# Kernel optimization log

Hardware: AMD Instinct MI355X
Metric: run time of the kernel (lower is better)

The kernel has to match this reference:

```python
import jax, jax.numpy as jnp
import numpy as np

LOG2 = 0.6931471805599453

def ssp(x):
    # shifted softplus, SchNet's standard activation
    return jax.nn.softplus(x) - LOG2

def setup_inputs() -> dict:
    key = jax.random.key(0)
    ks = jax.random.split(key, 8)
    B, A, N, G, F = 8, 1024, 64, 50, 128
    s = lambda fan_in: 1.0 / np.sqrt(fan_in)
    return {
        "x": jax.random.normal(ks[0], (B, A, F), jnp.float32),
        "pairwise_mask": jnp.ones((B, A, N), jnp.float32),
        "neighbors": jax.random.randint(ks[1], (B, A, N), 0, A),
        "f_ij": jax.random.uniform(ks[2], (B, A, N, G), jnp.float32),
        "W_f1": jax.random.normal(ks[3], (G, F), jnp.float32) * s(G),
        "b_f1": jnp.zeros((F,), jnp.float32),
        "W_f2": jax.random.normal(ks[4], (F, F), jnp.float32) * s(F),
        "b_f2": jnp.zeros((F,), jnp.float32),
        "W_in2f": jax.random.normal(ks[5], (F, F), jnp.float32) * s(F),
        "W_f2out": jax.random.normal(ks[6], (F, F), jnp.float32) * s(F),
        "b_f2out": jnp.zeros((F,), jnp.float32),
    }

def reference(x, pairwise_mask, neighbors, f_ij, W_f1, b_f1, W_f2, b_f2,
              W_in2f, W_f2out, b_f2out):
    B, A, N = neighbors.shape
    # filter network: Dense+ssp then Dense (no activation) -> [B,A,N,F]
    W = ssp(jnp.einsum('bang,gf->banf', f_ij, W_f1) + b_f1)
    W = jnp.einsum('banf,fk->bank', W, W_f2) + b_f2
    # neighbor gather: x[b, neighbors[b,a,n], :] -> [B,A,N,C]
    nbh = neighbors.reshape(B, A * N, 1)           # [B, A*N, 1]
    x_nbh = jnp.take_along_axis(x, nbh, axis=1)    # broadcast over C -> [B, A*N, C]
    x_nbh = x_nbh.reshape(B, A, N, -1)
    # in2f dense (no bias), filter multiply, masked sum over neighbor axis
    y = jnp.einsum('banc,cf->banf', x_nbh, W_in2f)
    y = y * W
    y = jnp.sum(y * pairwise_mask[..., None], axis=2)  # [B, A, F]
    # f2out dense with shifted-softplus activation
    y = ssp(jnp.einsum('baf,fo->bao', y, W_f2out) + b_f2out)
    return y
```

## Files before the change

### kernel.cpp

```cpp
#include <hip/hip_runtime.h>

#define B_ 8
#define A_ 1024
#define N_ 64
#define G_ 50
#define F_ 128
#define ATOMS 4

typedef __attribute__((ext_vector_type(8))) short bf16x8;
typedef __attribute__((ext_vector_type(4))) float f32x4;

__device__ __forceinline__ float sspf(float v) {
    return fmaxf(v, 0.f) + __logf(1.f + __expf(-fabsf(v))) - 0.69314718055994530942f;
}
__device__ __forceinline__ unsigned short f2bf(float f) {
    unsigned u = __float_as_uint(f);
    u += 0x7fffu + ((u >> 16) & 1u);
    return (unsigned short)(u >> 16);
}
__device__ __forceinline__ unsigned cvt_pk(float lo, float hi) {
    unsigned r;
    asm("v_cvt_pk_bf16_f32 %0, %1, %2" : "=v"(r) : "v"(lo), "v"(hi));
    return r;
}
__device__ __forceinline__ float red16(float p) {
    p += __int_as_float(__builtin_amdgcn_ds_swizzle(__float_as_int(p), 0x041F));
    p += __int_as_float(__builtin_amdgcn_ds_swizzle(__float_as_int(p), 0x081F));
    p += __int_as_float(__builtin_amdgcn_ds_swizzle(__float_as_int(p), 0x101F));
    p += __int_as_float(__builtin_amdgcn_ds_swizzle(__float_as_int(p), 0x201F));
    return p;
}

__global__ __launch_bounds__(256) void pack_all(
    const float* __restrict__ W1, const float* __restrict__ b1,
    const float* __restrict__ W2, const float* __restrict__ Wi,
    const float* __restrict__ Wo,
    unsigned short* __restrict__ P1, unsigned short* __restrict__ P2,
    unsigned short* __restrict__ Pi, unsigned short* __restrict__ Po)
{
    int blk = blockIdx.x;
    const float* W; const float* bias = nullptr; unsigned short* P; int K, id;
    if (blk < 32)       { W = W1; P = P1; K = 50;  id = blk * 256 + threadIdx.x; bias = b1; }
    else if (blk < 96)  { W = W2; P = P2; K = 128; id = (blk - 32) * 256 + threadIdx.x; }
    else if (blk < 160) { W = Wi; P = Pi; K = 128; id = (blk - 96) * 256 + threadIdx.x; }
    else                { W = Wo; P = Po; K = 128; id = (blk - 160) * 256 + threadIdx.x; }
    int i    = id & 7;
    int lane = (id >> 3) & 63;
    int nt   = (id >> 9) & 7;
    int ks   = id >> 12;
    int k = 32 * ks + 8 * (lane >> 4) + i;
    int f = 16 * nt + (lane & 15);
    float v = (k < K) ? W[k * F_ + f] : ((bias && k == K) ? bias[f] : 0.f);
    P[id] = f2bf(v);
}

template <bool ACT, bool OUT_BF16>
__global__ __launch_bounds__(64) void rowgemm_kernel(
    const float* Afp, const unsigned short* __restrict__ Bp,
    const float* __restrict__ bias, void* outv)
{
    const int l  = threadIdx.x;
    const int r0 = blockIdx.x * 16;
    const bf16x8* Bv = (const bf16x8*)Bp;

    f32x4 acc[8];
    #pragma unroll
    for (int nt = 0; nt < 8; ++nt) acc[nt] = f32x4{0.f, 0.f, 0.f, 0.f};

    const int arow = r0 + (l & 15);
    const int koff = (l >> 4) * 8;
    #pragma unroll
    for (int ks = 0; ks < 4; ++ks) {
        const float* ap = Afp + (size_t)arow * F_ + ks * 32 + koff;
        float4 a0 = *(const float4*)ap;
        float4 a1 = *(const float4*)(ap + 4);
        bf16x8 af;
        af[0] = (short)f2bf(a0.x); af[1] = (short)f2bf(a0.y);
        af[2] = (short)f2bf(a0.z); af[3] = (short)f2bf(a0.w);
        af[4] = (short)f2bf(a1.x); af[5] = (short)f2bf(a1.y);
        af[6] = (short)f2bf(a1.z); af[7] = (short)f2bf(a1.w);
        #pragma unroll
        for (int nt = 0; nt < 8; ++nt) {
            bf16x8 bf = Bv[(ks * 8 + nt) * 64 + l];
            acc[nt] = __builtin_amdgcn_mfma_f32_16x16x32_bf16(af, bf, acc[nt], 0, 0, 0);
        }
    }
    #pragma unroll
    for (int nt = 0; nt < 8; ++nt) {
        int f = nt * 16 + (l & 15);
        float bv = bias ? bias[f] : 0.f;
        #pragma unroll
        for (int r = 0; r < 4; ++r) {
            int orow = r0 + (l >> 4) * 4 + r;
            float v = acc[nt][r] + bv;
            if (ACT) v = sspf(v);
            if (OUT_BF16) ((unsigned short*)outv)[(size_t)orow * F_ + f] = f2bf(v);
            else          ((float*)outv)[(size_t)orow * F_ + f] = v;
        }
    }
}

__global__ __launch_bounds__(256, 3) void cfconv_main(
    const unsigned short* __restrict__ xt,
    const float* __restrict__ mask,
    const int*   __restrict__ nbr,
    const float* __restrict__ fij,
    const unsigned short* __restrict__ W1s,
    const unsigned short* __restrict__ W2s,
    const float* __restrict__ bf2,
    float* __restrict__ Y)
{
    const int ba0 = blockIdx.x * ATOMS;
    const int b   = ba0 >> 10;
    const int t   = threadIdx.x;
    const int w   = t >> 6;
    const int l   = t & 63;
    const int l16 = l & 15;
    const int q   = l >> 4;

    __shared__ unsigned short s_fp[2][4096];
    __shared__ unsigned short s_hp[8192];

    const bf16x8* w1v = (const bf16x8*)W1s;
    const bf16x8* w2v = (const bf16x8*)W2s;
    bf16x8 W1r[2][2], W2r[4][2];
    #pragma unroll
    for (int ks = 0; ks < 2; ++ks) {
        W1r[ks][0] = w1v[(ks * 8 + 2 * w + 0) * 64 + l];
        W1r[ks][1] = w1v[(ks * 8 + 2 * w + 1) * 64 + l];
    }
    #pragma unroll
    for (int ks = 0; ks < 4; ++ks) {
        W2r[ks][0] = w2v[(ks * 8 + 2 * w + 0) * 64 + l];
        W2r[ks][1] = w2v[(ks * 8 + 2 * w + 1) * 64 + l];
    }
    float4 b2r[2];
    b2r[0] = *(const float4*)(bf2 + 16 * (2 * w + 0) + 4 * q);
    b2r[1] = *(const float4*)(bf2 + 16 * (2 * w + 1) + 4 * q);

    int nbv[4]; float mkv[4];
    #pragma unroll
    for (int nt = 0; nt < 4; ++nt) {
        nbv[nt] = nbr[(size_t)ba0 * N_ + 16 * nt + l16];
        mkv[nt] = mask[(size_t)ba0 * N_ + 16 * nt + l16];
    }
    float2 fa[4], fb[4];
    {
        const float* frow = fij + (size_t)ba0 * (N_ * G_) + (16 * w + l16) * G_;
        #pragma unroll
        for (int j = 0; j < 4; ++j) fa[j] = *(const float2*)(frow + 8 * q + 2 * j);
        if (q < 2) {
            #pragma unroll
            for (int j = 0; j < 4; ++j) fb[j] = *(const float2*)(frow + 32 + 8 * q + 2 * j);
        } else if (q == 2) {
            fb[0] = *(const float2*)(frow + 48);
            fb[1] = float2{1.f, 0.f};
            fb[2] = float2{0.f, 0.f}; fb[3] = float2{0.f, 0.f};
        } else {
            #pragma unroll
            for (int j = 0; j < 4; ++j) fb[j] = float2{0.f, 0.f};
        }
    }
    uint2 xg[2][4];
    #pragma unroll
    for (int f2 = 0; f2 < 2; ++f2) {
        const int f0 = 16 * (2 * w + f2) + 4 * q;
        #pragma unroll
        for (int nt = 0; nt < 4; ++nt)
            xg[f2][nt] = *(const uint2*)(xt + ((size_t)(b << 10) + nbv[nt]) * F_ + f0);
    }
    {
        uint4 pk0, pk1;
        pk0.x = cvt_pk(fa[0].x, fa[0].y); pk0.y = cvt_pk(fa[1].x, fa[1].y);
        pk0.z = cvt_pk(fa[2].x, fa[2].y); pk0.w = cvt_pk(fa[3].x, fa[3].y);
        pk1.x = cvt_pk(fb[0].x, fb[0].y); pk1.y = cvt_pk(fb[1].x, fb[1].y);
        pk1.z = cvt_pk(fb[2].x, fb[2].y); pk1.w = cvt_pk(fb[3].x, fb[3].y);
        *(uint4*)(&s_fp[0][((w * 2 + 0) * 64 + l) * 8]) = pk0;
        *(uint4*)(&s_fp[0][((w * 2 + 1) * 64 + l) * 8]) = pk1;
    }
    __syncthreads();

    int nbv2[4]; float mkv2[4];

    #pragma unroll
    for (int i = 0; i < ATOMS; ++i) {
        const int ba = ba0 + i;
        const unsigned short* fp_cur = s_fp[i & 1];
        unsigned short* fp_nxt = s_fp[(i + 1) & 1];

        const bf16x8* fv = (const bf16x8*)fp_cur;
        f32x4 acc1[2][4];
        #pragma unroll
        for (int c = 0; c < 2; ++c)
            #pragma unroll
            for (int nt = 0; nt < 4; ++nt) acc1[c][nt] = f32x4{0.f, 0.f, 0.f, 0.f};
        #pragma unroll
        for (int ks = 0; ks < 2; ++ks) {
            bf16x8 bb[4];
            #pragma unroll
            for (int nt = 0; nt < 4; ++nt) bb[nt] = fv[(nt * 2 + ks) * 64 + l];
            #pragma unroll
            for (int nt = 0; nt < 4; ++nt) {
                acc1[0][nt] = __builtin_amdgcn_mfma_f32_16x16x32_bf16(W1r[ks][0], bb[nt], acc1[0][nt], 0, 0, 0);
                acc1[1][nt] = __builtin_amdgcn_mfma_f32_16x16x32_bf16(W1r[ks][1], bb[nt], acc1[1][nt], 0, 0, 0);
            }
        }

        if (i < ATOMS - 1) {
            const float* frow = fij + (size_t)(ba + 1) * (N_ * G_) + (16 * w + l16) * G_;
            #pragma unroll
            for (int j = 0; j < 4; ++j) fa[j] = *(const float2*)(frow + 8 * q + 2 * j);
            if (q < 2) {
                #pragma unroll
                for (int j = 0; j < 4; ++j) fb[j] = *(const float2*)(frow + 32 + 8 * q + 2 * j);
            } else if (q == 2) {
                fb[0] = *(const float2*)(frow + 48);
                fb[1] = float2{1.f, 0.f};
                fb[2] = float2{0.f, 0.f}; fb[3] = float2{0.f, 0.f};
            } else {
                #pragma unroll
                for (int j = 0; j < 4; ++j) fb[j] = float2{0.f, 0.f};
            }
            #pragma unroll
            for (int nt = 0; nt < 4; ++nt) {
                nbv2[nt] = nbr[(size_t)(ba + 1) * N_ + 16 * nt + l16];
                mkv2[nt] = mask[(size_t)(ba + 1) * N_ + 16 * nt + l16];
            }
        }

        #pragma unroll
        for (int ct2 = 0; ct2 < 2; ++ct2) {
            const int addr = ((w * 64 + 16 * (2 * ct2 + (q >> 1)) + l16) * 8 + 4 * (q & 1));
            #pragma unroll
            for (int nt = 0; nt < 4; ++nt) {
                float h0 = sspf(acc1[ct2][nt][0]);
                float h1 = sspf(acc1[ct2][nt][1]);
                float h2 = sspf(acc1[ct2][nt][2]);
                float h3 = sspf(acc1[ct2][nt][3]);
                uint2 pk;
                pk.x = cvt_pk(h0, h1);
                pk.y = cvt_pk(h2, h3);
                *(uint2*)(&s_hp[nt * 2048 + addr]) = pk;
            }
        }

        if (i < ATOMS - 1) {
            uint4 pk0, pk1;
            pk0.x = cvt_pk(fa[0].x, fa[0].y); pk0.y = cvt_pk(fa[1].x, fa[1].y);
            pk0.z = cvt_pk(fa[2].x, fa[2].y); pk0.w = cvt_pk(fa[3].x, fa[3].y);
            pk1.x = cvt_pk(fb[0].x, fb[0].y); pk1.y = cvt_pk(fb[1].x, fb[1].y);
            pk1.z = cvt_pk(fb[2].x, fb[2].y); pk1.w = cvt_pk(fb[3].x, fb[3].y);
            *(uint4*)(&fp_nxt[((w * 2 + 0) * 64 + l) * 8]) = pk0;
            *(uint4*)(&fp_nxt[((w * 2 + 1) * 64 + l) * 8]) = pk1;
        }
        __syncthreads();

        const bf16x8* hv = (const bf16x8*)s_hp;
        f32x4 acc2[2][4];
        #pragma unroll
        for (int c = 0; c < 2; ++c)
            #pragma unroll
            for (int nt = 0; nt < 4; ++nt) acc2[c][nt] = f32x4{0.f, 0.f, 0.f, 0.f};
        #pragma unroll
        for (int ks = 0; ks < 4; ++ks) {
            bf16x8 bb[4];
            #pragma unroll
            for (int nt = 0; nt < 4; ++nt) bb[nt] = hv[(nt * 4 + ks) * 64 + l];
            #pragma unroll
            for (int nt = 0; nt < 4; ++nt) {
                acc2[0][nt] = __builtin_amdgcn_mfma_f32_16x16x32_bf16(W2r[ks][0], bb[nt], acc2[0][nt], 0, 0, 0);
                acc2[1][nt] = __builtin_amdgcn_mfma_f32_16x16x32_bf16(W2r[ks][1], bb[nt], acc2[1][nt], 0, 0, 0);
            }
        }

        #pragma unroll
        for (int f2 = 0; f2 < 2; ++f2) {
            const float4 b2v = b2r[f2];
            float p0 = 0.f, p1 = 0.f, p2 = 0.f, p3 = 0.f;
            #pragma unroll
            for (int nt = 0; nt < 4; ++nt) {
                const float msk = mkv[nt];
                const uint2 xv = xg[f2][nt];
                const float x0 = __uint_as_float(xv.x << 16);
                const float x1 = __uint_as_float(xv.x & 0xffff0000u);
                const float x2 = __uint_as_float(xv.y << 16);
                const float x3 = __uint_as_float(xv.y & 0xffff0000u);
                p0 = fmaf(msk * (acc2[f2][nt][0] + b2v.x), x0, p0);
                p1 = fmaf(msk * (acc2[f2][nt][1] + b2v.y), x1, p1);
                p2 = fmaf(msk * (acc2[f2][nt][2] + b2v.z), x2, p2);
                p3 = fmaf(msk * (acc2[f2][nt][3] + b2v.w), x3, p3);
            }
            p0 = red16(p0); p1 = red16(p1); p2 = red16(p2); p3 = red16(p3);
            if (l16 == 0)
                *(float4*)(Y + (size_t)ba * F_ + 16 * (2 * w + f2) + 4 * q) = float4{p0, p1, p2, p3};
        }

        if (i < ATOMS - 1) {
            #pragma unroll
            for (int nt = 0; nt < 4; ++nt) { nbv[nt] = nbv2[nt]; mkv[nt] = mkv2[nt]; }
            #pragma unroll
            for (int f2 = 0; f2 < 2; ++f2) {
                const int f0 = 16 * (2 * w + f2) + 4 * q;
                #pragma unroll
                for (int nt = 0; nt < 4; ++nt)
                    xg[f2][nt] = *(const uint2*)(xt + ((size_t)(b << 10) + nbv[nt]) * F_ + f0);
            }
        }
        __syncthreads();
    }
}

extern "C" void kernel_launch(void* const* d_in, const int* in_sizes, int n_in,
                              void* d_out, int out_size, void* d_ws, size_t ws_size,
                              hipStream_t stream) {
    const float* x     = (const float*)d_in[0];
    const float* mask  = (const float*)d_in[1];
    const int*   nbr   = (const int*)d_in[2];
    const float* fij   = (const float*)d_in[3];
    const float* Wf1   = (const float*)d_in[4];
    const float* bf1   = (const float*)d_in[5];
    const float* Wf2   = (const float*)d_in[6];
    const float* bf2   = (const float*)d_in[7];
    const float* Win2f = (const float*)d_in[8];
    const float* Wout  = (const float*)d_in[9];
    const float* bout  = (const float*)d_in[10];
    float* out = (float*)d_out;

    char* ws = (char*)d_ws;
    unsigned short* W1p   = (unsigned short*)(ws);
    unsigned short* W2p   = (unsigned short*)(ws + 16384);
    unsigned short* Winp  = (unsigned short*)(ws + 49152);
    unsigned short* Woutp = (unsigned short*)(ws + 81920);
    unsigned short* xt    = (unsigned short*)(ws + 114688);

    pack_all<<<224, 256, 0, stream>>>(Wf1, bf1, Wf2, Win2f, Wout, W1p, W2p, Winp, Woutp);

    rowgemm_kernel<false, true><<<B_ * A_ / 16, 64, 0, stream>>>(x, Winp, nullptr, xt);

    cfconv_main<<<B_ * A_ / ATOMS, 256, 0, stream>>>(xt, mask, nbr, fij, W1p, W2p, bf2, out);

    rowgemm_kernel<true, false><<<B_ * A_ / 16, 64, 0, stream>>>(out, Woutp, bout, out);
}
```

Measured before the change: 91.83 us.

## Raise occupancy, single-buffer filter LDS, swizzle blocks, fold bias into MFMA, add setprio

Raises the launch-bounds occupancy hint from 3 to 5 waves and halves the f_ij LDS staging by using a single buffer, which needs an extra barrier between the layer-1 MFMAs and the overwrite. Blocks are remapped with an XCD-style swizzle (bid&7) so that neighboring atoms go to the same die, aiming at better L2 locality for the gathered x rows. The bias b_f2 now initialises the second GEMM's MFMA accumulator instead of being added in the epilogue, and the first k-step seeds with zero so no accumulators need clearing. s_setprio wraps the MFMA sections, and address math is simplified. The tighter register budget may cause spills.

```diff
diff --git a/kernel.cpp b/kernel.cpp
--- a/kernel.cpp
+++ b/kernel.cpp
@@ -100,7 +100,7 @@
     }
 }
 
-__global__ __launch_bounds__(256, 3) void cfconv_main(
+__global__ __launch_bounds__(256, 5) void cfconv_main(
     const unsigned short* __restrict__ xt,
     const float* __restrict__ mask,
     const int*   __restrict__ nbr,
@@ -110,16 +110,20 @@
     const float* __restrict__ bf2,
     float* __restrict__ Y)
 {
-    const int ba0 = blockIdx.x * ATOMS;
-    const int b   = ba0 >> 10;
+    const int bid = blockIdx.x;
+    const int swz = (bid & 7) * (2048 / 8) + (bid >> 3);
+    const int ba0 = swz * ATOMS;
     const int t   = threadIdx.x;
     const int w   = t >> 6;
     const int l   = t & 63;
     const int l16 = l & 15;
     const int q   = l >> 4;
 
-    __shared__ unsigned short s_fp[2][4096];
+    __shared__ unsigned short s_fp[4096];
     __shared__ unsigned short s_hp[8192];
+
+    const unsigned short* xt_b = xt + ((size_t)(ba0 >> 10) << 10) * F_;
+    const int xoff = 32 * w + 4 * q;
 
     const bf16x8* w1v = (const bf16x8*)W1s;
     const bf16x8* w2v = (const bf16x8*)W2s;
@@ -134,15 +138,23 @@
         W2r[ks][0] = w2v[(ks * 8 + 2 * w + 0) * 64 + l];
         W2r[ks][1] = w2v[(ks * 8 + 2 * w + 1) * 64 + l];
     }
-    float4 b2r[2];
-    b2r[0] = *(const float4*)(bf2 + 16 * (2 * w + 0) + 4 * q);
-    b2r[1] = *(const float4*)(bf2 + 16 * (2 * w + 1) + 4 * q);
+    f32x4 b2acc[2];
+    {
+        float4 t0 = *(const float4*)(bf2 + 16 * (2 * w + 0) + 4 * q);
+        float4 t1 = *(const float4*)(bf2 + 16 * (2 * w + 1) + 4 * q);
+        b2acc[0] = f32x4{t0.x, t0.y, t0.z, t0.w};
+        b2acc[1] = f32x4{t1.x, t1.y, t1.z, t1.w};
+    }
 
     int nbv[4]; float mkv[4];
-    #pragma unroll
-    for (int nt = 0; nt < 4; ++nt) {
-        nbv[nt] = nbr[(size_t)ba0 * N_ + 16 * nt + l16];
-        mkv[nt] = mask[(size_t)ba0 * N_ + 16 * nt + l16];
+    {
+        const int*   nb0 = nbr  + (size_t)ba0 * N_;
+        const float* mk0 = mask + (size_t)ba0 * N_;
+        #pragma unroll
+        for (int nt = 0; nt < 4; ++nt) {
+            nbv[nt] = nb0[16 * nt + l16];
+            mkv[nt] = mk0[16 * nt + l16];
+        }
     }
     float2 fa[4], fb[4];
     {
@@ -163,20 +175,18 @@
     }
     uint2 xg[2][4];
     #pragma unroll
-    for (int f2 = 0; f2 < 2; ++f2) {
-        const int f0 = 16 * (2 * w + f2) + 4 * q;
+    for (int f2 = 0; f2 < 2; ++f2)
         #pragma unroll
         for (int nt = 0; nt < 4; ++nt)
-            xg[f2][nt] = *(const uint2*)(xt + ((size_t)(b << 10) + nbv[nt]) * F_ + f0);
-    }
+            xg[f2][nt] = *(const uint2*)(xt_b + nbv[nt] * F_ + xoff + 16 * f2);
     {
         uint4 pk0, pk1;
         pk0.x = cvt_pk(fa[0].x, fa[0].y); pk0.y = cvt_pk(fa[1].x, fa[1].y);
         pk0.z = cvt_pk(fa[2].x, fa[2].y); pk0.w = cvt_pk(fa[3].x, fa[3].y);
         pk1.x = cvt_pk(fb[0].x, fb[0].y); pk1.y = cvt_pk(fb[1].x, fb[1].y);
         pk1.z = cvt_pk(fb[2].x, fb[2].y); pk1.w = cvt_pk(fb[3].x, fb[3].y);
-        *(uint4*)(&s_fp[0][((w * 2 + 0) * 64 + l) * 8]) = pk0;
-        *(uint4*)(&s_fp[0][((w * 2 + 1) * 64 + l) * 8]) = pk1;
+        *(uint4*)(&s_fp[((w * 2 + 0) * 64 + l) * 8]) = pk0;
+        *(uint4*)(&s_fp[((w * 2 + 1) * 64 + l) * 8]) = pk1;
     }
     __syncthreads();
 
@@ -185,26 +195,28 @@
     #pragma unroll
     for (int i = 0; i < ATOMS; ++i) {
         const int ba = ba0 + i;
-        const unsigned short* fp_cur = s_fp[i & 1];
-        unsigned short* fp_nxt = s_fp[(i + 1) & 1];
-
-        const bf16x8* fv = (const bf16x8*)fp_cur;
+
+        const bf16x8* fv = (const bf16x8*)s_fp;
         f32x4 acc1[2][4];
-        #pragma unroll
-        for (int c = 0; c < 2; ++c)
-            #pragma unroll
-            for (int nt = 0; nt < 4; ++nt) acc1[c][nt] = f32x4{0.f, 0.f, 0.f, 0.f};
-        #pragma unroll
-        for (int ks = 0; ks < 2; ++ks) {
+        __builtin_amdgcn_s_setprio(1);
+        {
             bf16x8 bb[4];
             #pragma unroll
-            for (int nt = 0; nt < 4; ++nt) bb[nt] = fv[(nt * 2 + ks) * 64 + l];
-            #pragma unroll
-            for (int nt = 0; nt < 4; ++nt) {
-                acc1[0][nt] = __builtin_amdgcn_mfma_f32_16x16x32_bf16(W1r[ks][0], bb[nt], acc1[0][nt], 0, 0, 0);
-                acc1[1][nt] = __builtin_amdgcn_mfma_f32_16x16x32_bf16(W1r[ks][1], bb[nt], acc1[1][nt], 0, 0, 0);
-            }
-        }
+            for (int nt = 0; nt < 4; ++nt) bb[nt] = fv[(nt * 2 + 0) * 64 + l];
+            #pragma unroll
+            for (int nt = 0; nt < 4; ++nt) {
+                acc1[0][nt] = __builtin_amdgcn_mfma_f32_16x16x32_bf16(W1r[0][0], bb[nt], f32x4{0.f,0.f,0.f,0.f}, 0, 0, 0);
+                acc1[1][nt] = __builtin_amdgcn_mfma_f32_16x16x32_bf16(W1r[0][1], bb[nt], f32x4{0.f,0.f,0.f,0.f}, 0, 0, 0);
+            }
+            #pragma unroll
+            for (int nt = 0; nt < 4; ++nt) bb[nt] = fv[(nt * 2 + 1) * 64 + l];
+            #pragma unroll
+            for (int nt = 0; nt < 4; ++nt) {
+                acc1[0][nt] = __builtin_amdgcn_mfma_f32_16x16x32_bf16(W1r[1][0], bb[nt], acc1[0][nt], 0, 0, 0);
+                acc1[1][nt] = __builtin_amdgcn_mfma_f32_16x16x32_bf16(W1r[1][1], bb[nt], acc1[1][nt], 0, 0, 0);
+            }
+        }
+        __builtin_amdgcn_s_setprio(0);
 
         if (i < ATOMS - 1) {
             const float* frow = fij + (size_t)(ba + 1) * (N_ * G_) + (16 * w + l16) * G_;
@@ -221,10 +233,12 @@
                 #pragma unroll
                 for (int j = 0; j < 4; ++j) fb[j] = float2{0.f, 0.f};
             }
-            #pragma unroll
-            for (int nt = 0; nt < 4; ++nt) {
-                nbv2[nt] = nbr[(size_t)(ba + 1) * N_ + 16 * nt + l16];
-                mkv2[nt] = mask[(size_t)(ba + 1) * N_ + 16 * nt + l16];
+            const int*   nb1 = nbr  + (size_t)(ba + 1) * N_;
+            const float* mk1 = mask + (size_t)(ba + 1) * N_;
+            #pragma unroll
+            for (int nt = 0; nt < 4; ++nt) {
+                nbv2[nt] = nb1[16 * nt + l16];
+                mkv2[nt] = mk1[16 * nt + l16];
             }
         }
 
@@ -243,6 +257,7 @@
                 *(uint2*)(&s_hp[nt * 2048 + addr]) = pk;
             }
         }
+        __syncthreads();
 
         if (i < ATOMS - 1) {
             uint4 pk0, pk1;
@@ -250,32 +265,37 @@
             pk0.z = cvt_pk(fa[2].x, fa[2].y); pk0.w = cvt_pk(fa[3].x, fa[3].y);
             pk1.x = cvt_pk(fb[0].x, fb[0].y); pk1.y = cvt_pk(fb[1].x, fb[1].y);
             pk1.z = cvt_pk(fb[2].x, fb[2].y); pk1.w = cvt_pk(fb[3].x, fb[3].y);
-            *(uint4*)(&fp_nxt[((w * 2 + 0) * 64 + l) * 8]) = pk0;
-            *(uint4*)(&fp_nxt[((w * 2 + 1) * 64 + l) * 8]) = pk1;
-        }
-        __syncthreads();
+            *(uint4*)(&s_fp[((w * 2 + 0) * 64 + l) * 8]) = pk0;
+            *(uint4*)(&s_fp[((w * 2 + 1) * 64 + l) * 8]) = pk1;
+        }
 
         const bf16x8* hv = (const bf16x8*)s_hp;
         f32x4 acc2[2][4];
-        #pragma unroll
-        for (int c = 0; c < 2; ++c)
-            #pragma unroll
-            for (int nt = 0; nt < 4; ++nt) acc2[c][nt] = f32x4{0.f, 0.f, 0.f, 0.f};
-        #pragma unroll
-        for (int ks = 0; ks < 4; ++ks) {
+        __builtin_amdgcn_s_setprio(1);
+        {
             bf16x8 bb[4];
             #pragma unroll
-            for (int nt = 0; nt < 4; ++nt) bb[nt] = hv[(nt * 4 + ks) * 64 + l];
-            #pragma unroll
-            for (int nt = 0; nt < 4; ++nt) {
-                acc2[0][nt] = __builtin_amdgcn_mfma_f32_16x16x32_bf16(W2r[ks][0], bb[nt], acc2[0][nt], 0, 0, 0);
-                acc2[1][nt] = __builtin_amdgcn_mfma_f32_16x16x32_bf16(W2r[ks][1], bb[nt], acc2[1][nt], 0, 0, 0);
-            }
-        }
+            for (int nt = 0; nt < 4; ++nt) bb[nt] = hv[(nt * 4 + 0) * 64 + l];
+            #pragma unroll
+            for (int nt = 0; nt < 4; ++nt) {
+                acc2[0][nt] = __builtin_amdgcn_mfma_f32_16x16x32_bf16(W2r[0][0], bb[nt], b2acc[0], 0, 0, 0);
+                acc2[1][nt] = __builtin_amdgcn_mfma_f32_16x16x32_bf16(W2r[0][1], bb[nt], b2acc[1], 0, 0, 0);
+            }
+            #pragma unroll
+            for (int ks = 1; ks < 4; ++ks) {
+                #pragma unroll
+                for (int nt = 0; nt < 4; ++nt) bb[nt] = hv[(nt * 4 + ks) * 64 + l];
+                #pragma unroll
+                for (int nt = 0; nt < 4; ++nt) {
+                    acc2[0][nt] = __builtin_amdgcn_mfma_f32_16x16x32_bf16(W2r[ks][0], bb[nt], acc2[0][nt], 0, 0, 0);
+                    acc2[1][nt] = __builtin_amdgcn_mfma_f32_16x16x32_bf16(W2r[ks][1], bb[nt], acc2[1][nt], 0, 0, 0);
+                }
+            }
+        }
+        __builtin_amdgcn_s_setprio(0);
 
         #pragma unroll
         for (int f2 = 0; f2 < 2; ++f2) {
-            const float4 b2v = b2r[f2];
             float p0 = 0.f, p1 = 0.f, p2 = 0.f, p3 = 0.f;
             #pragma unroll
             for (int nt = 0; nt < 4; ++nt) {
@@ -285,10 +305,10 @@
                 const float x1 = __uint_as_float(xv.x & 0xffff0000u);
                 const float x2 = __uint_as_float(xv.y << 16);
                 const float x3 = __uint_as_float(xv.y & 0xffff0000u);
-                p0 = fmaf(msk * (acc2[f2][nt][0] + b2v.x), x0, p0);
-                p1 = fmaf(msk * (acc2[f2][nt][1] + b2v.y), x1, p1);
-                p2 = fmaf(msk * (acc2[f2][nt][2] + b2v.z), x2, p2);
-                p3 = fmaf(msk * (acc2[f2][nt][3] + b2v.w), x3, p3);
+                p0 = fmaf(msk * acc2[f2][nt][0], x0, p0);
+                p1 = fmaf(msk * acc2[f2][nt][1], x1, p1);
+                p2 = fmaf(msk * acc2[f2][nt][2], x2, p2);
+                p3 = fmaf(msk * acc2[f2][nt][3], x3, p3);
             }
             p0 = red16(p0); p1 = red16(p1); p2 = red16(p2); p3 = red16(p3);
             if (l16 == 0)
@@ -299,12 +319,10 @@
             #pragma unroll
             for (int nt = 0; nt < 4; ++nt) { nbv[nt] = nbv2[nt]; mkv[nt] = mkv2[nt]; }
             #pragma unroll
-            for (int f2 = 0; f2 < 2; ++f2) {
-                const int f0 = 16 * (2 * w + f2) + 4 * q;
+            for (int f2 = 0; f2 < 2; ++f2)
                 #pragma unroll
                 for (int nt = 0; nt < 4; ++nt)
-                    xg[f2][nt] = *(const uint2*)(xt + ((size_t)(b << 10) + nbv[nt]) * F_ + f0);
-            }
+                    xg[f2][nt] = *(const uint2*)(xt_b + nbv[nt] * F_ + xoff + 16 * f2);
         }
         __syncthreads();
     }
```

New measurement: 169.1 us. 1.84x slower.
